# Kernel optimization log

Hardware: AMD Instinct MI355X
Metric: run time of the kernel (lower is better)

Reference implementation:

```python
import jax, jax.numpy as jnp
import numpy as np

N, P, S, CORE, H, HEADS, B = 49152, 256, 256, 192, 256, 8, 1
D = H // HEADS  # head_dim = 32
EPS = 1e-5


def setup_inputs() -> dict:
    key = jax.random.key(0)
    ks = jax.random.split(key, 8)
    x = jax.random.normal(ks[0], (B, N, H), dtype=jnp.float32)
    # cores tile all N nodes exactly once (KMeans-like partition), plus random overlap ring
    core = jnp.arange(N, dtype=jnp.int32).reshape(P, CORE)
    ov = jax.random.randint(ks[1], (P, S - CORE), 0, N, dtype=jnp.int32)
    patch_idx = jnp.concatenate([core, ov], axis=1)                      # [P,S]
    core_mask = jnp.concatenate(
        [jnp.ones((P, CORE), bool), jnp.zeros((P, S - CORE), bool)], axis=1)  # [P,S]
    def w(k):
        return jax.random.normal(k, (H, H), dtype=jnp.float32) * 0.02
    return dict(
        x=x, patch_idx=patch_idx, core_mask=core_mask,
        Wq=w(ks[2]), bq=jnp.zeros((H,), jnp.float32),
        Wk=w(ks[3]), bk=jnp.zeros((H,), jnp.float32),
        Wv=w(ks[4]), bv=jnp.zeros((H,), jnp.float32),
        Wo=w(ks[5]), bo=jnp.zeros((H,), jnp.float32),
        ln_g=jnp.ones((H,), jnp.float32), ln_b=jnp.zeros((H,), jnp.float32),
    )


def reference(x, patch_idx, core_mask, Wq, bq, Wk, bk, Wv, bv, Wo, bo, ln_g, ln_b):
    # x: [B,N,H]; patch_idx: [P,S] int; core_mask: [P,S] bool
    px = x[:, patch_idx]                                   # gather -> [B,P,S,H]
    def proj(W, b):
        return (px @ W.T + b).reshape(B, P, S, HEADS, D)
    Q, K, V = proj(Wq, bq), proj(Wk, bk), proj(Wv, bv)
    scores = jnp.einsum('bpihd,bpjhd->bphij', Q, K) / jnp.sqrt(jnp.float32(D))
    attn = jax.nn.softmax(scores, axis=-1)                 # dropout is identity in eval
    att = jnp.einsum('bphij,bpjhd->bpihd', attn, V).reshape(B, P, S, H)
    out = att @ Wo.T + bo                                  # [B,P,S,H]
    # scatter-add only core slots back to nodes, track update counts
    contrib = jnp.where(core_mask[None, :, :, None], out, 0.0).reshape(B, P * S, H)
    flat = patch_idx.reshape(-1)
    acc = jnp.zeros((B, N, H), x.dtype).at[:, flat].add(contrib)
    cnt = jnp.zeros((N,), x.dtype).at[flat].add(core_mask.reshape(-1).astype(x.dtype))
    acc = acc / jnp.clip(cnt, 1.0)[None, :, None]
    # residual + LayerNorm (biased variance, as torch)
    y = x + acc
    mu = jnp.mean(y, axis=-1, keepdims=True)
    var = jnp.var(y, axis=-1, keepdims=True)
    return (y - mu) / jnp.sqrt(var + EPS) * ln_g + ln_b
```

## Files before the change

kernel.cpp:

```cpp
#include <hip/hip_runtime.h>

#define PP 256
#define SS 256
#define CORE_ 192
#define HH 256
#define NHEAD 8
#define DD 32

typedef __attribute__((ext_vector_type(4))) float f32x4;
typedef __attribute__((ext_vector_type(8))) short s8v;
typedef __attribute__((ext_vector_type(4))) short s4v;

__device__ __forceinline__ float bf2f(unsigned short u) {
    union { unsigned int i; float f; } c; c.i = ((unsigned int)u) << 16; return c.f;
}
__device__ __forceinline__ unsigned short f2bf(float f) {
    union { float f; unsigned int i; } c; c.f = f;
    unsigned int i = c.i;
    return (unsigned short)((i + 0x7fffu + ((i >> 16) & 1u)) >> 16);
}

#define SW(row, chunk) ((chunk) ^ (((row) >> 1) & 3))

__global__ __launch_bounds__(256) void k_qkv(
    const float* __restrict__ x, const int* __restrict__ pidx,
    const float* __restrict__ Wq, const float* __restrict__ bq,
    const float* __restrict__ Wk, const float* __restrict__ bk,
    const float* __restrict__ Wv, const float* __restrict__ bv,
    unsigned short* __restrict__ qkv) {
    int p = blockIdx.x, mt = blockIdx.y, ng = blockIdx.z;
    if (ng == 0 && mt == 3) return;
    const float* W    = (ng == 0) ? Wq : (ng == 1) ? Wk : Wv;
    const float* bias = (ng == 0) ? bq : (ng == 1) ? bk : bv;
    __shared__ unsigned short As[64][32];
    __shared__ unsigned short Bs[256][32];
    int tid = threadIdx.x;
    int wave = tid >> 6, lane = tid & 63;
    int g = lane >> 4, c0 = lane & 15;
    f32x4 acc[4][4] = {};
    int arow = tid >> 2, aseg = tid & 3;
    int node = pidx[p * SS + mt * 64 + arow];
    const float* asrc = x + (size_t)node * HH + aseg * 8;

    for (int k0 = 0; k0 < HH; k0 += 32) {
        float4 v0 = *(const float4*)(asrc + k0);
        float4 v1 = *(const float4*)(asrc + k0 + 4);
        s8v aw;
        aw[0] = (short)f2bf(v0.x); aw[1] = (short)f2bf(v0.y);
        aw[2] = (short)f2bf(v0.z); aw[3] = (short)f2bf(v0.w);
        aw[4] = (short)f2bf(v1.x); aw[5] = (short)f2bf(v1.y);
        aw[6] = (short)f2bf(v1.z); aw[7] = (short)f2bf(v1.w);
        *(s8v*)&As[arow][SW(arow, aseg) * 8] = aw;
        int k4 = tid & 7;
        int nb = tid >> 3;
#pragma unroll
        for (int pass = 0; pass < 8; ++pass) {
            int n = nb + pass * 32;
            float4 v = *(const float4*)(W + (size_t)n * HH + k0 + k4 * 4);
            s4v bw;
            bw[0] = (short)f2bf(v.x); bw[1] = (short)f2bf(v.y);
            bw[2] = (short)f2bf(v.z); bw[3] = (short)f2bf(v.w);
            *(s4v*)&Bs[n][SW(n, k4 >> 1) * 8 + (k4 & 1) * 4] = bw;
        }
        __syncthreads();
        s8v af[4], bfv[4];
#pragma unroll
        for (int m2 = 0; m2 < 4; ++m2) {
            int r = m2 * 16 + c0;
            af[m2] = *(const s8v*)&As[r][SW(r, g) * 8];
        }
#pragma unroll
        for (int nt = 0; nt < 4; ++nt) {
            int r = wave * 64 + nt * 16 + c0;
            bfv[nt] = *(const s8v*)&Bs[r][SW(r, g) * 8];
        }
#pragma unroll
        for (int m2 = 0; m2 < 4; ++m2)
#pragma unroll
            for (int nt = 0; nt < 4; ++nt)
                acc[m2][nt] = __builtin_amdgcn_mfma_f32_16x16x32_bf16(
                    af[m2], bfv[nt], acc[m2][nt], 0, 0, 0);
        __syncthreads();
    }
#pragma unroll
    for (int nt = 0; nt < 4; ++nt) {
        int ncol = wave * 64 + nt * 16 + c0;
        float bv_ = bias[ncol];
#pragma unroll
        for (int m2 = 0; m2 < 4; ++m2)
#pragma unroll
            for (int r = 0; r < 4; ++r) {
                int srow = mt * 64 + m2 * 16 + g * 4 + r;
                qkv[((size_t)p * SS + srow) * 768 + ng * 256 + ncol] =
                    f2bf(acc[m2][nt][r] + bv_);
            }
    }
}

__global__ __launch_bounds__(256) void k_attn(
    const unsigned short* __restrict__ qkv, unsigned short* __restrict__ att) {
    int p = blockIdx.x, h = blockIdx.y;
    __shared__ unsigned short Ks[256][32];
    __shared__ unsigned short Vt[32][256];
    __shared__ unsigned short Pb[4][16][256];
    int tid = threadIdx.x;
    int wave = tid >> 6, lane = tid & 63;
    int g = lane >> 4, c0 = lane & 15;

    {
        int chunk = tid & 3, rb = tid >> 2;
#pragma unroll
        for (int pass = 0; pass < 4; ++pass) {
            int row = rb + pass * 64;
            const unsigned short* kb =
                qkv + ((size_t)p * SS + row) * 768 + 256 + h * DD + chunk * 8;
            s8v kv = *(const s8v*)kb;
            s8v vv = *(const s8v*)(kb + 256);
            *(s8v*)&Ks[row][SW(row, chunk) * 8] = kv;
            int cj = row >> 3, jo = row & 7;
#pragma unroll
            for (int e = 0; e < 8; ++e) {
                int d = chunk * 8 + e;
                Vt[d][((cj ^ ((d >> 1) & 7)) << 3) + jo] = (unsigned short)vv[e];
            }
        }
    }
    __syncthreads();

    const float scale = 0.17677669529663687f;
    int cs = (c0 >> 1) & 7;

    for (int mi = 0; mi < 3; ++mi) {
        int q0 = (wave * 3 + mi) * 16;
        s8v qa = *(const s8v*)(qkv + ((size_t)p * SS + q0 + c0) * 768 + h * DD + g * 8);
        f32x4 sacc[16];
#pragma unroll
        for (int jt = 0; jt < 16; ++jt) {
            int row = jt * 16 + c0;
            s8v kf = *(const s8v*)&Ks[row][SW(row, g) * 8];
            sacc[jt] = __builtin_amdgcn_mfma_f32_16x16x32_bf16(
                qa, kf, f32x4{0.f, 0.f, 0.f, 0.f}, 0, 0, 0);
        }
        float linv[4];
#pragma unroll
        for (int r = 0; r < 4; ++r) {
            float mx = sacc[0][r];
#pragma unroll
            for (int jt = 1; jt < 16; ++jt) mx = fmaxf(mx, sacc[jt][r]);
#pragma unroll
            for (int off = 1; off < 16; off <<= 1)
                mx = fmaxf(mx, __shfl_xor(mx, off, 64));
            float sum = 0.f;
#pragma unroll
            for (int jt = 0; jt < 16; ++jt) {
                float e = __expf((sacc[jt][r] - mx) * scale);
                sacc[jt][r] = e;
                sum += e;
            }
#pragma unroll
            for (int off = 1; off < 16; off <<= 1)
                sum += __shfl_xor(sum, off, 64);
            linv[r] = 1.f / sum;
            int q = g * 4 + r;
            int qs = (q >> 1) & 7;
            unsigned short* prow = &Pb[wave][q][0];
#pragma unroll
            for (int jt = 0; jt < 16; ++jt) {
                int j0 = jt * 2 + (c0 >> 3);
                prow[((j0 ^ qs) << 3) + (c0 & 7)] = (unsigned short)f2bf(sacc[jt][r]);
            }
        }
        asm volatile("s_waitcnt lgkmcnt(0)" ::: "memory");
        __builtin_amdgcn_sched_barrier(0);
        f32x4 oacc[2] = {f32x4{0.f, 0.f, 0.f, 0.f}, f32x4{0.f, 0.f, 0.f, 0.f}};
#pragma unroll
        for (int kt = 0; kt < 8; ++kt) {
            s8v pa = *(const s8v*)&Pb[wave][c0][(((kt * 4 + g) ^ cs) << 3)];
#pragma unroll
            for (int nt = 0; nt < 2; ++nt) {
                int d = nt * 16 + c0;
                s8v vb = *(const s8v*)&Vt[d][(((kt * 4 + g) ^ ((d >> 1) & 7)) << 3)];
                oacc[nt] = __builtin_amdgcn_mfma_f32_16x16x32_bf16(
                    pa, vb, oacc[nt], 0, 0, 0);
            }
        }
        asm volatile("s_waitcnt lgkmcnt(0)" ::: "memory");
        __builtin_amdgcn_sched_barrier(0);
#pragma unroll
        for (int nt = 0; nt < 2; ++nt)
#pragma unroll
            for (int r = 0; r < 4; ++r) {
                int q = g * 4 + r;
                att[((size_t)p * SS + q0 + q) * HH + h * DD + nt * 16 + c0] =
                    f2bf(oacc[nt][r] * linv[r]);
            }
    }
}

__global__ __launch_bounds__(256) void k_out(
    const unsigned short* __restrict__ att, const float* __restrict__ x,
    const float* __restrict__ Wo, const float* __restrict__ bo,
    const float* __restrict__ ln_g, const float* __restrict__ ln_b,
    float* __restrict__ out) {
    int p = blockIdx.x, mb = blockIdx.y;
    __shared__ unsigned short As[64][32];
    __shared__ unsigned short Bs[256][32];
    int tid = threadIdx.x;
    int wave = tid >> 6, lane = tid & 63;
    int g = lane >> 4, c0 = lane & 15;
    f32x4 acc[16] = {};
    int arow = tid >> 2, aseg = tid & 3;
    const unsigned short* asrc =
        att + ((size_t)p * SS + mb * 64 + arow) * HH + aseg * 8;
    int k4 = tid & 7;
    int nb = tid >> 3;

    for (int k0 = 0; k0 < HH; k0 += 32) {
        *(s8v*)&As[arow][SW(arow, aseg) * 8] = *(const s8v*)(asrc + k0);
#pragma unroll
        for (int pass = 0; pass < 8; ++pass) {
            int n = nb + pass * 32;
            float4 v = *(const float4*)(Wo + (size_t)n * HH + k0 + k4 * 4);
            s4v bw;
            bw[0] = (short)f2bf(v.x); bw[1] = (short)f2bf(v.y);
            bw[2] = (short)f2bf(v.z); bw[3] = (short)f2bf(v.w);
            *(s4v*)&Bs[n][SW(n, k4 >> 1) * 8 + (k4 & 1) * 4] = bw;
        }
        __syncthreads();
        int ar = wave * 16 + c0;
        s8v af = *(const s8v*)&As[ar][SW(ar, g) * 8];
#pragma unroll
        for (int nt = 0; nt < 16; ++nt) {
            int r = nt * 16 + c0;
            s8v bfv = *(const s8v*)&Bs[r][SW(r, g) * 8];
            acc[nt] = __builtin_amdgcn_mfma_f32_16x16x32_bf16(af, bfv, acc[nt], 0, 0, 0);
        }
        __syncthreads();
    }
    int srow0 = mb * 64 + wave * 16 + g * 4;
    float sum[4] = {0, 0, 0, 0}, ssq[4] = {0, 0, 0, 0};
#pragma unroll
    for (int nt = 0; nt < 16; ++nt) {
        int col = nt * 16 + c0;
        float bov = bo[col];
#pragma unroll
        for (int r = 0; r < 4; ++r) {
            size_t node = (size_t)p * CORE_ + srow0 + r;
            float v = acc[nt][r] + bov + x[node * HH + col];
            acc[nt][r] = v;
            sum[r] += v; ssq[r] += v * v;
        }
    }
#pragma unroll
    for (int off = 1; off < 16; off <<= 1) {
#pragma unroll
        for (int r = 0; r < 4; ++r) {
            sum[r] += __shfl_xor(sum[r], off, 64);
            ssq[r] += __shfl_xor(ssq[r], off, 64);
        }
    }
#pragma unroll
    for (int r = 0; r < 4; ++r) {
        float mu = sum[r] * (1.f / HH);
        float var = ssq[r] * (1.f / HH) - mu * mu;
        float rstd = rsqrtf(var + 1e-5f);
        size_t node = (size_t)p * CORE_ + srow0 + r;
#pragma unroll
        for (int nt = 0; nt < 16; ++nt) {
            int col = nt * 16 + c0;
            out[node * HH + col] = (acc[nt][r] - mu) * rstd * ln_g[col] + ln_b[col];
        }
    }
}

extern "C" void kernel_launch(void* const* d_in, const int* in_sizes, int n_in,
                              void* d_out, int out_size, void* d_ws, size_t ws_size,
                              hipStream_t stream) {
    const float* x   = (const float*)d_in[0];
    const int* pidx  = (const int*)d_in[1];
    const float* Wq  = (const float*)d_in[3];
    const float* bq  = (const float*)d_in[4];
    const float* Wk  = (const float*)d_in[5];
    const float* bk  = (const float*)d_in[6];
    const float* Wv  = (const float*)d_in[7];
    const float* bv  = (const float*)d_in[8];
    const float* Wo  = (const float*)d_in[9];
    const float* bo  = (const float*)d_in[10];
    const float* lng = (const float*)d_in[11];
    const float* lnb = (const float*)d_in[12];

    unsigned short* qkv = (unsigned short*)d_ws;
    unsigned short* att = qkv + (size_t)PP * SS * 768;

    k_qkv<<<dim3(PP, 4, 3), 256, 0, stream>>>(x, pidx, Wq, bq, Wk, bk, Wv, bv, qkv);
    k_attn<<<dim3(PP, NHEAD), 256, 0, stream>>>(qkv, att);
    k_out<<<dim3(PP, 3), 256, 0, stream>>>(att, x, Wo, bo, lng, lnb, (float*)d_out);
}
```

Measured before the change: 164.8 us.

## Pre-convert weights to bf16 once and keep the gathered A tile resident across QKV projections

Adds a prep kernel that converts Wq/Wk/Wv/Wo to bf16 and packs the biases into a workspace buffer, so the GEMM kernels load bf16 weights directly instead of converting fp32 each tile. k_qkv now gathers and converts each 64-row block of x into LDS once and loops over all Q/K/V column groups, replacing the separate z-dimension blocks that each re-gathered x. The att buffer is compacted to core rows only. This trades fewer blocks per grid and a larger LDS footprint, which may lower occupancy, plus an extra kernel launch.

```diff
diff --git a/kernel.cpp b/kernel.cpp
--- a/kernel.cpp
+++ b/kernel.cpp
@@ -21,79 +21,109 @@
 }
 
 #define SW(row, chunk) ((chunk) ^ (((row) >> 1) & 3))
+#define ASW(row, s) ((s) ^ ((row) & 7) ^ (((s) >> 3) & 7))
+
+__global__ __launch_bounds__(256) void k_prep(
+    const float* __restrict__ Wq, const float* __restrict__ Wk,
+    const float* __restrict__ Wv, const float* __restrict__ Wo,
+    const float* __restrict__ bq, const float* __restrict__ bk,
+    const float* __restrict__ bv,
+    unsigned short* __restrict__ Wb, float* __restrict__ bb) {
+    int bid = blockIdx.x, tid = threadIdx.x;
+    if (bid >= 256) {
+        int which = bid - 256;
+        const float* b = which == 0 ? bq : which == 1 ? bk : bv;
+        bb[which * 256 + tid] = b[tid];
+        return;
+    }
+    int i = bid * 256 + tid;
+    int row = i >> 6;
+    int col4 = (i & 63) * 4;
+    const float* src = row < 256 ? Wq : row < 512 ? Wk : row < 768 ? Wv : Wo;
+    float4 v = *(const float4*)(src + (size_t)(row & 255) * 256 + col4);
+    s4v w;
+    w[0] = (short)f2bf(v.x); w[1] = (short)f2bf(v.y);
+    w[2] = (short)f2bf(v.z); w[3] = (short)f2bf(v.w);
+    *(s4v*)(Wb + (size_t)row * 256 + col4) = w;
+}
 
 __global__ __launch_bounds__(256) void k_qkv(
     const float* __restrict__ x, const int* __restrict__ pidx,
-    const float* __restrict__ Wq, const float* __restrict__ bq,
-    const float* __restrict__ Wk, const float* __restrict__ bk,
-    const float* __restrict__ Wv, const float* __restrict__ bv,
+    const unsigned short* __restrict__ Wb, const float* __restrict__ bb,
     unsigned short* __restrict__ qkv) {
-    int p = blockIdx.x, mt = blockIdx.y, ng = blockIdx.z;
-    if (ng == 0 && mt == 3) return;
-    const float* W    = (ng == 0) ? Wq : (ng == 1) ? Wk : Wv;
-    const float* bias = (ng == 0) ? bq : (ng == 1) ? bk : bv;
-    __shared__ unsigned short As[64][32];
-    __shared__ unsigned short Bs[256][32];
+    int p = blockIdx.x, mt = blockIdx.y;
+    __shared__ unsigned short As[64][256];
+    __shared__ unsigned short Bs[192][32];
     int tid = threadIdx.x;
     int wave = tid >> 6, lane = tid & 63;
     int g = lane >> 4, c0 = lane & 15;
-    f32x4 acc[4][4] = {};
-    int arow = tid >> 2, aseg = tid & 3;
-    int node = pidx[p * SS + mt * 64 + arow];
-    const float* asrc = x + (size_t)node * HH + aseg * 8;
-
-    for (int k0 = 0; k0 < HH; k0 += 32) {
-        float4 v0 = *(const float4*)(asrc + k0);
-        float4 v1 = *(const float4*)(asrc + k0 + 4);
-        s8v aw;
-        aw[0] = (short)f2bf(v0.x); aw[1] = (short)f2bf(v0.y);
-        aw[2] = (short)f2bf(v0.z); aw[3] = (short)f2bf(v0.w);
-        aw[4] = (short)f2bf(v1.x); aw[5] = (short)f2bf(v1.y);
-        aw[6] = (short)f2bf(v1.z); aw[7] = (short)f2bf(v1.w);
-        *(s8v*)&As[arow][SW(arow, aseg) * 8] = aw;
-        int k4 = tid & 7;
-        int nb = tid >> 3;
-#pragma unroll
-        for (int pass = 0; pass < 8; ++pass) {
-            int n = nb + pass * 32;
-            float4 v = *(const float4*)(W + (size_t)n * HH + k0 + k4 * 4);
-            s4v bw;
-            bw[0] = (short)f2bf(v.x); bw[1] = (short)f2bf(v.y);
-            bw[2] = (short)f2bf(v.z); bw[3] = (short)f2bf(v.w);
-            *(s4v*)&Bs[n][SW(n, k4 >> 1) * 8 + (k4 & 1) * 4] = bw;
-        }
-        __syncthreads();
-        s8v af[4], bfv[4];
-#pragma unroll
-        for (int m2 = 0; m2 < 4; ++m2) {
-            int r = m2 * 16 + c0;
-            af[m2] = *(const s8v*)&As[r][SW(r, g) * 8];
-        }
-#pragma unroll
-        for (int nt = 0; nt < 4; ++nt) {
-            int r = wave * 64 + nt * 16 + c0;
-            bfv[nt] = *(const s8v*)&Bs[r][SW(r, g) * 8];
-        }
-#pragma unroll
-        for (int m2 = 0; m2 < 4; ++m2)
-#pragma unroll
-            for (int nt = 0; nt < 4; ++nt)
-                acc[m2][nt] = __builtin_amdgcn_mfma_f32_16x16x32_bf16(
-                    af[m2], bfv[nt], acc[m2][nt], 0, 0, 0);
-        __syncthreads();
-    }
-#pragma unroll
-    for (int nt = 0; nt < 4; ++nt) {
-        int ncol = wave * 64 + nt * 16 + c0;
-        float bv_ = bias[ncol];
-#pragma unroll
-        for (int m2 = 0; m2 < 4; ++m2)
-#pragma unroll
-            for (int r = 0; r < 4; ++r) {
-                int srow = mt * 64 + m2 * 16 + g * 4 + r;
-                qkv[((size_t)p * SS + srow) * 768 + ng * 256 + ncol] =
-                    f2bf(acc[m2][nt][r] + bv_);
-            }
+
+    {
+        int row = tid >> 2;
+        int sb = (tid & 3) * 8;
+        int node = pidx[p * SS + mt * 64 + row];
+        const float* src = x + (size_t)node * HH;
+#pragma unroll
+        for (int i = 0; i < 8; ++i) {
+            int s = sb + i;
+            float4 a = *(const float4*)(src + s * 8);
+            float4 b = *(const float4*)(src + s * 8 + 4);
+            s8v w;
+            w[0] = (short)f2bf(a.x); w[1] = (short)f2bf(a.y);
+            w[2] = (short)f2bf(a.z); w[3] = (short)f2bf(a.w);
+            w[4] = (short)f2bf(b.x); w[5] = (short)f2bf(b.y);
+            w[6] = (short)f2bf(b.z); w[7] = (short)f2bf(b.w);
+            *(s8v*)&As[row][ASW(row, s) * 8] = w;
+        }
+    }
+    __syncthreads();
+
+    for (int q = 0; q < 4; ++q) {
+        if (mt == 3 && q == 0) continue;
+        f32x4 acc[4][3] = {};
+        for (int ks = 0; ks < 8; ++ks) {
+#pragma unroll
+            for (int j = 0; j < 3; ++j) {
+                int task = tid + 256 * j;
+                int nr = task >> 2, sl = task & 3;
+                s8v w = *(const s8v*)(Wb + (size_t)(q * 192 + nr) * 256 + ks * 32 + sl * 8);
+                *(s8v*)&Bs[nr][SW(nr, sl) * 8] = w;
+            }
+            __syncthreads();
+            s8v af[4];
+#pragma unroll
+            for (int m2 = 0; m2 < 4; ++m2) {
+                int r = m2 * 16 + c0;
+                af[m2] = *(const s8v*)&As[r][ASW(r, ks * 4 + g) * 8];
+            }
+#pragma unroll
+            for (int nt = 0; nt < 3; ++nt) {
+                int T = q * 12 + wave * 3 + nt;
+                if (mt == 3 && T < 16) continue;
+                int nr = (wave * 3 + nt) * 16 + c0;
+                s8v bf = *(const s8v*)&Bs[nr][SW(nr, g) * 8];
+#pragma unroll
+                for (int m2 = 0; m2 < 4; ++m2)
+                    acc[m2][nt] = __builtin_amdgcn_mfma_f32_16x16x32_bf16(
+                        af[m2], bf, acc[m2][nt], 0, 0, 0);
+            }
+            __syncthreads();
+        }
+#pragma unroll
+        for (int nt = 0; nt < 3; ++nt) {
+            int T = q * 12 + wave * 3 + nt;
+            if (mt == 3 && T < 16) continue;
+            int col = T * 16 + c0;
+            float bv_ = bb[col];
+#pragma unroll
+            for (int m2 = 0; m2 < 4; ++m2)
+#pragma unroll
+                for (int r = 0; r < 4; ++r) {
+                    int srow = mt * 64 + m2 * 16 + g * 4 + r;
+                    qkv[((size_t)p * SS + srow) * 768 + col] =
+                        f2bf(acc[m2][nt][r] + bv_);
+                }
+        }
     }
 }
 
@@ -161,9 +191,9 @@
             for (int off = 1; off < 16; off <<= 1)
                 sum += __shfl_xor(sum, off, 64);
             linv[r] = 1.f / sum;
-            int q = g * 4 + r;
-            int qs = (q >> 1) & 7;
-            unsigned short* prow = &Pb[wave][q][0];
+            int qq = g * 4 + r;
+            int qs = (qq >> 1) & 7;
+            unsigned short* prow = &Pb[wave][qq][0];
 #pragma unroll
             for (int jt = 0; jt < 16; ++jt) {
                 int j0 = jt * 2 + (c0 >> 3);
@@ -190,8 +220,8 @@
         for (int nt = 0; nt < 2; ++nt)
 #pragma unroll
             for (int r = 0; r < 4; ++r) {
-                int q = g * 4 + r;
-                att[((size_t)p * SS + q0 + q) * HH + h * DD + nt * 16 + c0] =
+                int qq = g * 4 + r;
+                att[((size_t)p * CORE_ + q0 + qq) * HH + h * DD + nt * 16 + c0] =
                     f2bf(oacc[nt][r] * linv[r]);
             }
     }
@@ -199,7 +229,7 @@
 
 __global__ __launch_bounds__(256) void k_out(
     const unsigned short* __restrict__ att, const float* __restrict__ x,
-    const float* __restrict__ Wo, const float* __restrict__ bo,
+    const unsigned short* __restrict__ Wb, const float* __restrict__ bo,
     const float* __restrict__ ln_g, const float* __restrict__ ln_b,
     float* __restrict__ out) {
     int p = blockIdx.x, mb = blockIdx.y;
@@ -211,20 +241,16 @@
     f32x4 acc[16] = {};
     int arow = tid >> 2, aseg = tid & 3;
     const unsigned short* asrc =
-        att + ((size_t)p * SS + mb * 64 + arow) * HH + aseg * 8;
-    int k4 = tid & 7;
-    int nb = tid >> 3;
+        att + ((size_t)p * CORE_ + mb * 64 + arow) * HH + aseg * 8;
 
     for (int k0 = 0; k0 < HH; k0 += 32) {
         *(s8v*)&As[arow][SW(arow, aseg) * 8] = *(const s8v*)(asrc + k0);
 #pragma unroll
-        for (int pass = 0; pass < 8; ++pass) {
-            int n = nb + pass * 32;
-            float4 v = *(const float4*)(Wo + (size_t)n * HH + k0 + k4 * 4);
-            s4v bw;
-            bw[0] = (short)f2bf(v.x); bw[1] = (short)f2bf(v.y);
-            bw[2] = (short)f2bf(v.z); bw[3] = (short)f2bf(v.w);
-            *(s4v*)&Bs[n][SW(n, k4 >> 1) * 8 + (k4 & 1) * 4] = bw;
+        for (int j = 0; j < 4; ++j) {
+            int task = tid + 256 * j;
+            int nr = task >> 2, sl = task & 3;
+            s8v w = *(const s8v*)(Wb + (size_t)(768 + nr) * 256 + k0 + sl * 8);
+            *(s8v*)&Bs[nr][SW(nr, sl) * 8] = w;
         }
         __syncthreads();
         int ar = wave * 16 + c0;
@@ -291,8 +317,11 @@
 
     unsigned short* qkv = (unsigned short*)d_ws;
     unsigned short* att = qkv + (size_t)PP * SS * 768;
-
-    k_qkv<<<dim3(PP, 4, 3), 256, 0, stream>>>(x, pidx, Wq, bq, Wk, bk, Wv, bv, qkv);
+    unsigned short* Wb  = att + (size_t)PP * CORE_ * HH;
+    float* bb = (float*)(Wb + 1024 * 256);
+
+    k_prep<<<259, 256, 0, stream>>>(Wq, Wk, Wv, Wo, bq, bk, bv, Wb, bb);
+    k_qkv<<<dim3(PP, 4), 256, 0, stream>>>(x, pidx, Wb, bb, qkv);
     k_attn<<<dim3(PP, NHEAD), 256, 0, stream>>>(qkv, att);
-    k_out<<<dim3(PP, 3), 256, 0, stream>>>(att, x, Wo, bo, lng, lnb, (float*)d_out);
-}
+    k_out<<<dim3(PP, 3), 256, 0, stream>>>(att, x, Wb, bo, lng, lnb, (float*)d_out);
+}
```

New measurement: 173.1 us. 5.1% more time.
